# Performance work log

Measured on AMD Instinct MI355X. Metric: run time of the kernel, lower is better.

## Reference

```python
import jax, jax.numpy as jnp
import numpy as np

HEAD_NUM = 16
EMBED = 1024

def setup_inputs() -> dict:
    key = jax.random.key(0)
    k1, k2, k3 = jax.random.split(key, 3)
    x = jax.random.normal(k1, (2, 2048, EMBED), dtype=jnp.float32)
    W_qkv = jax.random.normal(k2, (3 * EMBED, EMBED), dtype=jnp.float32) * (EMBED ** -0.5)
    W_out = jax.random.normal(k3, (EMBED, EMBED), dtype=jnp.float32) * (EMBED ** -0.5)
    return {"x": x, "W_qkv": W_qkv, "W_out": W_out}

def reference(x, W_qkv, W_out):
    b, t, E = x.shape
    h = HEAD_NUM
    d = E // h
    dk = (E / h) ** 0.5
    qkv = x @ W_qkv.T  # [b, t, 3E]
    # einops 'b t (d k h) -> k b h t d' with k=3, h=head_num (d outermost in the split)
    qkv = qkv.reshape(b, t, d, 3, h).transpose(3, 0, 4, 1, 2)  # [3, b, h, t, d]
    q, k, v = qkv[0], qkv[1], qkv[2]
    energy = jnp.einsum('bhid,bhjd->bhij', q, k) / dk  # [b, h, t, t]
    attn = jax.nn.softmax(energy, axis=-1)
    out = jnp.einsum('bhij,bhjd->bhid', attn, v)  # [b, h, t, d]
    out = out.transpose(0, 2, 1, 3).reshape(b, t, E)  # 'b h t d -> b t (h d)'
    return out @ W_out.T
```

## Files before the change

### kernel.cpp

```cpp
#include <hip/hip_runtime.h>
#include <hip/hip_bf16.h>


#define HEADS 16
#define EMB   1024
#define HDIM  64
#define BB    2
#define TT    2048
#define QSCALE 0.18033688011112042f

typedef __attribute__((ext_vector_type(8)))  short      bf16x8;
typedef __attribute__((ext_vector_type(8)))  _Float16   f16x8;
typedef __attribute__((ext_vector_type(4)))  float      f32x4;
typedef __attribute__((ext_vector_type(16))) float      f32x16;
typedef __attribute__((ext_vector_type(4)))  unsigned   u32x4;

__device__ __forceinline__ unsigned short f2bf(float f) {
    __hip_bfloat16 h = __float2bfloat16(f);
    return __builtin_bit_cast(unsigned short, h);
}
__device__ __forceinline__ float fexp2(float x) {
#if __has_builtin(__builtin_amdgcn_exp2f)
    return __builtin_amdgcn_exp2f(x);
#else
    return exp2f(x);
#endif
}
__device__ __forceinline__ unsigned pkrtz(float a, float b) {
    auto r = __builtin_amdgcn_cvt_pkrtz(a, b);
    return __builtin_bit_cast(unsigned, r);
}
__device__ __forceinline__ unsigned short f2h(float f) {
    return (unsigned short)(pkrtz(f, 0.f) & 0xffffu);
}
__device__ __forceinline__ float h2f(unsigned short u) {
    return (float)__builtin_bit_cast(_Float16, u);
}
__device__ __forceinline__ void gload_lds16(const void* g, void* l) {
    __builtin_amdgcn_global_load_lds(
        (const __attribute__((address_space(1))) void*)g,
        (__attribute__((address_space(3))) void*)l, 16, 0, 0);
}
__device__ __forceinline__ int swzi(int row, int blk) {
    return row * 64 + ((blk ^ (row & 7)) << 3);
}
__device__ __forceinline__ void pl32swap(unsigned& a, unsigned& b) {
    asm("v_permlane32_swap_b32 %0, %1" : "+v"(a), "+v"(b));
}

__global__ __launch_bounds__(256)
void conv_bf16(const float* __restrict__ src, unsigned short* __restrict__ dst,
               int n8) {
    int i = blockIdx.x * 256 + threadIdx.x;
    if (i >= n8) return;
    const float4 v0 = ((const float4*)src)[i * 2];
    const float4 v1 = ((const float4*)src)[i * 2 + 1];
    ushort4 a, b;
    a.x = f2bf(v0.x); a.y = f2bf(v0.y); a.z = f2bf(v0.z); a.w = f2bf(v0.w);
    b.x = f2bf(v1.x); b.y = f2bf(v1.y); b.z = f2bf(v1.z); b.w = f2bf(v1.w);
    ((ushort4*)dst)[i * 2]     = a;
    ((ushort4*)dst)[i * 2 + 1] = b;
}

template<int PERM>
__global__ __launch_bounds__(256)
void convw(const float* __restrict__ src, unsigned short* __restrict__ dst) {
    const int np = blockIdx.x;
    const int ns = PERM ? ((np & 63) * 48 + (np >> 10) * 16 + ((np >> 6) & 15))
                        : np;
    const float4 v = ((const float4*)(src + (size_t)ns * 1024))[threadIdx.x];
    ushort4 u;
    u.x = f2bf(v.x); u.y = f2bf(v.y); u.z = f2bf(v.z); u.w = f2bf(v.w);
    ((ushort4*)(dst + (size_t)np * 1024))[threadIdx.x] = u;
}

template<int EPI>
__global__ __launch_bounds__(256)
void gemm_bf16(const unsigned short* __restrict__ Ag,
               const unsigned short* __restrict__ Wg,
               float* __restrict__ Cout,
               unsigned short* __restrict__ QKb,
               unsigned short* __restrict__ Vt) {
    __shared__ __align__(16) unsigned short Ab[128 * 64];
    __shared__ __align__(16) unsigned short Wb[128 * 64];

    const int tid = threadIdx.x, lane = tid & 63, w = tid >> 6;
    const int n0 = blockIdx.x * 128, m0 = blockIdx.y * 128;
    const int wn = (w >> 1) * 64, wm = (w & 1) * 64;
    const int r16 = lane & 15, g = lane >> 4;

    f32x4 acc[4][4];
    #pragma unroll
    for (int i = 0; i < 4; ++i)
        #pragma unroll
        for (int j = 0; j < 4; ++j)
            acc[i][j] = (f32x4){0.f, 0.f, 0.f, 0.f};

    const int srl = lane >> 3;
    const int scb = lane & 7;

    for (int kt = 0; kt < 16; ++kt) {
        __syncthreads();
        const int k0 = kt * 64;
        #pragma unroll
        for (int i = 0; i < 4; ++i) {
            const int row = w * 32 + i * 8 + srl;
            const int cbs = (scb ^ (row & 7)) << 3;
            gload_lds16(Ag + (size_t)(m0 + row) * 1024 + k0 + cbs,
                        Ab + (size_t)(w * 32 + i * 8) * 64);
            gload_lds16(Wg + (size_t)(n0 + row) * 1024 + k0 + cbs,
                        Wb + (size_t)(w * 32 + i * 8) * 64);
        }
        __syncthreads();

        #pragma unroll
        for (int ks = 0; ks < 2; ++ks) {
            bf16x8 xf[4];
            #pragma unroll
            for (int mi = 0; mi < 4; ++mi)
                xf[mi] = *(const bf16x8*)&Ab[swzi(wm + mi * 16 + r16, ks * 4 + g)];
            #pragma unroll
            for (int ni = 0; ni < 4; ++ni) {
                const bf16x8 wf = *(const bf16x8*)&Wb[swzi(wn + ni * 16 + r16, ks * 4 + g)];
                #pragma unroll
                for (int mi = 0; mi < 4; ++mi)
                    acc[ni][mi] = __builtin_amdgcn_mfma_f32_16x16x32_bf16(
                        wf, xf[mi], acc[ni][mi], 0, 0, 0);
            }
        }
    }

    const int gq = g * 4;
    if (EPI == 0) {
        #pragma unroll
        for (int ni = 0; ni < 4; ++ni)
            #pragma unroll
            for (int mi = 0; mi < 4; ++mi) {
                const int m = m0 + wm + mi * 16 + r16;
                *(f32x4*)&Cout[(size_t)m * 1024 + (n0 + wn + ni * 16 + gq)] =
                    acc[ni][mi];
            }
    } else if (n0 < 2048) {
        #pragma unroll
        for (int ni = 0; ni < 4; ++ni) {
            const float qs = (n0 + wn + ni * 16) < 1024 ? QSCALE : 1.0f;
            #pragma unroll
            for (int mi = 0; mi < 4; ++mi) {
                const int m  = m0 + wm + mi * 16 + r16;
                const int np = n0 + wn + ni * 16 + gq;
                ushort4 u;
                u.x = f2bf(acc[ni][mi][0] * qs); u.y = f2bf(acc[ni][mi][1] * qs);
                u.z = f2bf(acc[ni][mi][2] * qs); u.w = f2bf(acc[ni][mi][3] * qs);
                *(ushort4*)&QKb[(size_t)m * 2048 + np] = u;
            }
        }
    } else {
        const int b = m0 >> 11, t0 = m0 & 2047;
        #pragma unroll
        for (int ni = 0; ni < 4; ++ni)
            #pragma unroll
            for (int mi = 0; mi < 4; ++mi) {
                const int t   = t0 + wm + mi * 16 + r16;
                const int nv0 = (n0 - 2048) + wn + ni * 16 + gq;
                #pragma unroll
                for (int j = 0; j < 4; ++j) {
                    const int nv = nv0 + j, h = nv >> 6, d = nv & 63;
                    Vt[(((size_t)(b * HEADS + h)) * HDIM + d) * TT + t] =
                        f2h(acc[ni][mi][j]);
                }
            }
    }
}

__global__ __launch_bounds__(256)
void attn32(const unsigned short* __restrict__ QKb,
            const unsigned short* __restrict__ Vt,
            unsigned short* __restrict__ PO0,
            unsigned short* __restrict__ PO1,
            float* __restrict__ PL0,
            float* __restrict__ PL1) {
    __shared__ __align__(16) unsigned short Ks[2][64 * 64];
    __shared__ __align__(16) unsigned short Vs[2][64 * 64];

    const int tid = threadIdx.x, lane = tid & 63, w = tid >> 6;
    const int l31 = lane & 31, hi = lane >> 5;
    const int qt = blockIdx.x & 15, kh = blockIdx.x >> 4;
    const int h = blockIdx.y, b = blockIdx.z;
    const int kbase = kh * 1024;
    const unsigned short* Vsrc = Vt + (size_t)(b * HEADS + h) * HDIM * TT;
    unsigned short* PO = kh ? PO1 : PO0;
    float*          PL = kh ? PL1 : PL0;

    bf16x8 qf[4];
    {
        const unsigned short* qrow =
            QKb + ((size_t)(b * TT + qt * 128 + w * 32 + l31)) * 2048 + h * HDIM;
        #pragma unroll
        for (int dc = 0; dc < 4; ++dc)
            qf[dc] = *(const bf16x8*)(qrow + dc * 16 + hi * 8);
    }

    const f32x16 zz = {};
    f32x16 o0 = {}, o1 = {};
    float lrun = 0.f;

    const int srl = lane >> 3;
    const int scb = lane & 7;

#define STAGEKV(BUF, J0)                                                         \
    do {                                                                         \
        _Pragma("unroll")                                                        \
        for (int i = 0; i < 2; ++i) {                                            \
            const int rl  = w * 16 + i * 8 + srl;                                \
            const int cbs = (scb ^ (rl & 7)) << 3;                               \
            gload_lds16(QKb + (size_t)(b * TT + (J0) + rl) * 2048 + 1024 +       \
                            h * HDIM + cbs,                                      \
                        &Ks[BUF][(w * 16 + i * 8) * 64]);                        \
            gload_lds16(Vsrc + (size_t)rl * TT + (J0) + cbs,                     \
                        &Vs[BUF][(w * 16 + i * 8) * 64]);                        \
        }                                                                        \
    } while (0)

    STAGEKV(0, kbase);

    for (int jt = 0; jt < 16; ++jt) {
        const int bb = jt & 1;
        __syncthreads();
        if (jt < 15) STAGEKV(bb ^ 1, kbase + (jt + 1) * 64);

        f32x16 st0, st1;
        __builtin_amdgcn_s_setprio(1);
        #pragma unroll
        for (int dc = 0; dc < 4; ++dc) {
            const bf16x8 ka0 = *(const bf16x8*)&Ks[bb][swzi(l31,      dc * 2 + hi)];
            const bf16x8 ka1 = *(const bf16x8*)&Ks[bb][swzi(32 + l31, dc * 2 + hi)];
            if (dc == 0) {
                st0 = __builtin_amdgcn_mfma_f32_32x32x16_bf16(ka0, qf[0], zz, 0, 0, 0);
                st1 = __builtin_amdgcn_mfma_f32_32x32x16_bf16(ka1, qf[0], zz, 0, 0, 0);
            } else {
                st0 = __builtin_amdgcn_mfma_f32_32x32x16_bf16(ka0, qf[dc], st0, 0, 0, 0);
                st1 = __builtin_amdgcn_mfma_f32_32x32x16_bf16(ka1, qf[dc], st1, 0, 0, 0);
            }
        }
        __builtin_amdgcn_s_setprio(0);

        float p[32];
        #pragma unroll
        for (int j = 0; j < 16; ++j) {
            p[j]      = fexp2(st0[j]);
            p[16 + j] = fexp2(st1[j]);
        }
        {
            float t[16];
            #pragma unroll
            for (int j = 0; j < 16; ++j) t[j] = p[j] + p[16 + j];
            #pragma unroll
            for (int j = 0; j < 8; ++j) t[j] += t[j + 8];
            #pragma unroll
            for (int j = 0; j < 4; ++j) t[j] += t[j + 4];
            lrun += (t[0] + t[1]) + (t[2] + t[3]);
        }

        unsigned wd[16];
        #pragma unroll
        for (int c = 0; c < 4; ++c) {
            wd[c * 2 + 0]     = pkrtz(p[4 * c + 0],      p[4 * c + 1]);
            wd[c * 2 + 1]     = pkrtz(p[4 * c + 2],      p[4 * c + 3]);
            wd[8 + c * 2 + 0] = pkrtz(p[16 + 4 * c + 0], p[16 + 4 * c + 1]);
            wd[8 + c * 2 + 1] = pkrtz(p[16 + 4 * c + 2], p[16 + 4 * c + 3]);
        }
        f16x8 pa[4];
        #pragma unroll
        for (int f = 0; f < 4; ++f) {
            unsigned w0 = wd[f * 4 + 0], w2 = wd[f * 4 + 2];
            pl32swap(w0, w2);
            unsigned w1 = wd[f * 4 + 1], w3 = wd[f * 4 + 3];
            pl32swap(w1, w3);
            const u32x4 fv = {w0, w1, w2, w3};
            pa[f] = __builtin_bit_cast(f16x8, fv);
        }

        __builtin_amdgcn_s_setprio(1);
        #pragma unroll
        for (int f = 0; f < 4; ++f) {
            const f16x8 vb0 = *(const f16x8*)&Vs[bb][swzi(l31,      f * 2 + hi)];
            const f16x8 vb1 = *(const f16x8*)&Vs[bb][swzi(32 + l31, f * 2 + hi)];
            o0 = __builtin_amdgcn_mfma_f32_32x32x16_f16(pa[f], vb0, o0, 0, 0, 0);
            o1 = __builtin_amdgcn_mfma_f32_32x32x16_f16(pa[f], vb1, o1, 0, 0, 0);
        }
        __builtin_amdgcn_s_setprio(0);
    }
#undef STAGEKV

    lrun += __shfl_xor(lrun, 32);
    const float inv = 1.0f / lrun;
    #pragma unroll
    for (int r = 0; r < 16; ++r) {
        const int qr = (r & 3) + 8 * (r >> 2) + 4 * hi;
        const float ir = __shfl(inv, qr);
        const int q = qt * 128 + w * 32 + qr;
        unsigned short* dst = PO + ((size_t)(b * TT + q)) * EMB + h * HDIM + l31;
        dst[0]  = f2h(o0[r] * ir);
        dst[32] = f2h(o1[r] * ir);
    }
    if (!hi) {
        const int q = qt * 128 + w * 32 + l31;
        PL[((size_t)(b * HEADS + h)) * TT + q] = lrun;
    }
}

__global__ __launch_bounds__(256)
void merge_attn(const unsigned short* __restrict__ PO0,
                const unsigned short* __restrict__ PO1,
                const float* __restrict__ PL0,
                const float* __restrict__ PL1,
                unsigned short* __restrict__ AOb) {
    const int i = blockIdx.x * 256 + threadIdx.x;
    const int tg  = i >> 8;
    const int col = (i & 255) * 4;
    const int h   = col >> 6;
    const int b   = tg >> 11, t = tg & 2047;

    const float la = PL0[((size_t)(b * HEADS + h)) * TT + t];
    const float lb = PL1[((size_t)(b * HEADS + h)) * TT + t];
    const float inv = 1.0f / (la + lb);
    const float wa = la * inv, wb = lb * inv;

    const ushort4 a = ((const ushort4*)PO0)[i];
    const ushort4 c = ((const ushort4*)PO1)[i];
    ushort4 o;
    o.x = f2bf(h2f(a.x) * wa + h2f(c.x) * wb);
    o.y = f2bf(h2f(a.y) * wa + h2f(c.y) * wb);
    o.z = f2bf(h2f(a.z) * wa + h2f(c.z) * wb);
    o.w = f2bf(h2f(a.w) * wa + h2f(c.w) * wb);
    ((ushort4*)AOb)[i] = o;
}

extern "C" void kernel_launch(void* const* d_in, const int* in_sizes, int n_in,
                              void* d_out, int out_size, void* d_ws, size_t ws_size,
                              hipStream_t stream) {
    const float* x    = (const float*)d_in[0];
    const float* Wqkv = (const float*)d_in[1];
    const float* Wout = (const float*)d_in[2];
    float* out = (float*)d_out;

    unsigned short* Wqb = (unsigned short*)d_ws;
    unsigned short* Wob = Wqb + 3145728;
    unsigned short* xb  = Wob + 1048576;
    unsigned short* QKb = xb  + 4194304;
    unsigned short* Vt  = QKb + 8388608;
    unsigned short* PO0 = Vt  + 4194304;
    unsigned short* PO1 = PO0 + 4194304;
    float*          PL0 = (float*)(PO1 + 4194304);
    float*          PL1 = PL0 + 65536;
    unsigned short* AOb = xb;

    conv_bf16<<<2048, 256, 0, stream>>>(x, xb, 524288);
    convw<1><<<3072, 256, 0, stream>>>(Wqkv, Wqb);
    convw<0><<<1024, 256, 0, stream>>>(Wout, Wob);

    gemm_bf16<1><<<dim3(24, 32), 256, 0, stream>>>(xb, Wqb, nullptr, QKb, Vt);

    attn32<<<dim3(32, 16, 2), 256, 0, stream>>>(QKb, Vt, PO0, PO1, PL0, PL1);

    merge_attn<<<4096, 256, 0, stream>>>(PO0, PO1, PL0, PL1, AOb);

    gemm_bf16<0><<<dim3(8, 32), 256, 0, stream>>>(AOb, Wob, out, nullptr, nullptr);
}
```

Measured before the change: 143.4 us.

## Hoist staging pointers, split softmax-PV per half, raise occupancy hint

The attention kernel now precomputes its K/V global and LDS staging addresses once and advances them by a constant stride, instead of recomputing swizzled addresses every tile. The exp/pack/PV stage is split into two halves (one per 32-key score block), so each half's PV MFMAs can start sooner and fewer probability values are live at once. The launch bounds now request 4 blocks per SM to cap register use. The intent is lower address arithmetic and register pressure and better overlap of exp with MFMA; the cap risks spills or the compiler reordering the schedule differently.

```diff
diff --git a/kernel.cpp b/kernel.cpp
--- a/kernel.cpp
+++ b/kernel.cpp
@@ -172,7 +172,7 @@
     }
 }
 
-__global__ __launch_bounds__(256)
+__global__ __launch_bounds__(256, 4)
 void attn32(const unsigned short* __restrict__ QKb,
             const unsigned short* __restrict__ Vt,
             unsigned short* __restrict__ PO0,
@@ -206,91 +206,95 @@
 
     const int srl = lane >> 3;
     const int scb = lane & 7;
-
-#define STAGEKV(BUF, J0)                                                         \
-    do {                                                                         \
-        _Pragma("unroll")                                                        \
-        for (int i = 0; i < 2; ++i) {                                            \
-            const int rl  = w * 16 + i * 8 + srl;                                \
-            const int cbs = (scb ^ (rl & 7)) << 3;                               \
-            gload_lds16(QKb + (size_t)(b * TT + (J0) + rl) * 2048 + 1024 +       \
-                            h * HDIM + cbs,                                      \
-                        &Ks[BUF][(w * 16 + i * 8) * 64]);                        \
-            gload_lds16(Vsrc + (size_t)rl * TT + (J0) + cbs,                     \
-                        &Vs[BUF][(w * 16 + i * 8) * 64]);                        \
-        }                                                                        \
+    const int cbs = (scb ^ srl) << 3;
+    const int rl0 = w * 16 + srl, rl1 = rl0 + 8;
+    const unsigned short* kp0 =
+        QKb + (size_t)(b * TT + kbase + rl0) * 2048 + 1024 + h * HDIM + cbs;
+    const unsigned short* kp1 = kp0 + (size_t)8 * 2048;
+    const unsigned short* vp0 = Vsrc + (size_t)rl0 * TT + kbase + cbs;
+    const unsigned short* vp1 = vp0 + (size_t)8 * TT;
+    unsigned short* const kd0 = &Ks[0][(w * 16) * 64];
+    unsigned short* const kd1 = &Ks[1][(w * 16) * 64];
+    unsigned short* const vd0 = &Vs[0][(w * 16) * 64];
+    unsigned short* const vd1 = &Vs[1][(w * 16) * 64];
+
+#define STAGE(KD, VD)                                                  \
+    do {                                                               \
+        gload_lds16(kp0, (KD));        gload_lds16(kp1, (KD) + 512);   \
+        gload_lds16(vp0, (VD));        gload_lds16(vp1, (VD) + 512);   \
+        kp0 += 64 * 2048; kp1 += 64 * 2048; vp0 += 64; vp1 += 64;      \
     } while (0)
 
-    STAGEKV(0, kbase);
+    STAGE(kd0, vd0);
 
     for (int jt = 0; jt < 16; ++jt) {
         const int bb = jt & 1;
         __syncthreads();
-        if (jt < 15) STAGEKV(bb ^ 1, kbase + (jt + 1) * 64);
-
-        f32x16 st0, st1;
+        if (jt < 15) {
+            if (bb) STAGE(kd0, vd0); else STAGE(kd1, vd1);
+        }
+        const unsigned short* KsB = &Ks[bb][0];
+        const unsigned short* VsB = &Vs[bb][0];
+
+        f32x16 stA, stB;
         __builtin_amdgcn_s_setprio(1);
         #pragma unroll
         for (int dc = 0; dc < 4; ++dc) {
-            const bf16x8 ka0 = *(const bf16x8*)&Ks[bb][swzi(l31,      dc * 2 + hi)];
-            const bf16x8 ka1 = *(const bf16x8*)&Ks[bb][swzi(32 + l31, dc * 2 + hi)];
+            const bf16x8 kaA = *(const bf16x8*)&KsB[swzi(l31,      dc * 2 + hi)];
+            const bf16x8 kaB = *(const bf16x8*)&KsB[swzi(32 + l31, dc * 2 + hi)];
             if (dc == 0) {
-                st0 = __builtin_amdgcn_mfma_f32_32x32x16_bf16(ka0, qf[0], zz, 0, 0, 0);
-                st1 = __builtin_amdgcn_mfma_f32_32x32x16_bf16(ka1, qf[0], zz, 0, 0, 0);
+                stA = __builtin_amdgcn_mfma_f32_32x32x16_bf16(kaA, qf[0], zz, 0, 0, 0);
+                stB = __builtin_amdgcn_mfma_f32_32x32x16_bf16(kaB, qf[0], zz, 0, 0, 0);
             } else {
-                st0 = __builtin_amdgcn_mfma_f32_32x32x16_bf16(ka0, qf[dc], st0, 0, 0, 0);
-                st1 = __builtin_amdgcn_mfma_f32_32x32x16_bf16(ka1, qf[dc], st1, 0, 0, 0);
+                stA = __builtin_amdgcn_mfma_f32_32x32x16_bf16(kaA, qf[dc], stA, 0, 0, 0);
+                stB = __builtin_amdgcn_mfma_f32_32x32x16_bf16(kaB, qf[dc], stB, 0, 0, 0);
             }
         }
         __builtin_amdgcn_s_setprio(0);
 
-        float p[32];
-        #pragma unroll
-        for (int j = 0; j < 16; ++j) {
-            p[j]      = fexp2(st0[j]);
-            p[16 + j] = fexp2(st1[j]);
-        }
-        {
-            float t[16];
-            #pragma unroll
-            for (int j = 0; j < 16; ++j) t[j] = p[j] + p[16 + j];
-            #pragma unroll
-            for (int j = 0; j < 8; ++j) t[j] += t[j + 8];
-            #pragma unroll
-            for (int j = 0; j < 4; ++j) t[j] += t[j + 4];
-            lrun += (t[0] + t[1]) + (t[2] + t[3]);
-        }
-
-        unsigned wd[16];
-        #pragma unroll
-        for (int c = 0; c < 4; ++c) {
-            wd[c * 2 + 0]     = pkrtz(p[4 * c + 0],      p[4 * c + 1]);
-            wd[c * 2 + 1]     = pkrtz(p[4 * c + 2],      p[4 * c + 3]);
-            wd[8 + c * 2 + 0] = pkrtz(p[16 + 4 * c + 0], p[16 + 4 * c + 1]);
-            wd[8 + c * 2 + 1] = pkrtz(p[16 + 4 * c + 2], p[16 + 4 * c + 3]);
-        }
-        f16x8 pa[4];
-        #pragma unroll
-        for (int f = 0; f < 4; ++f) {
-            unsigned w0 = wd[f * 4 + 0], w2 = wd[f * 4 + 2];
-            pl32swap(w0, w2);
-            unsigned w1 = wd[f * 4 + 1], w3 = wd[f * 4 + 3];
-            pl32swap(w1, w3);
-            const u32x4 fv = {w0, w1, w2, w3};
-            pa[f] = __builtin_bit_cast(f16x8, fv);
-        }
-
-        __builtin_amdgcn_s_setprio(1);
-        #pragma unroll
-        for (int f = 0; f < 4; ++f) {
-            const f16x8 vb0 = *(const f16x8*)&Vs[bb][swzi(l31,      f * 2 + hi)];
-            const f16x8 vb1 = *(const f16x8*)&Vs[bb][swzi(32 + l31, f * 2 + hi)];
-            o0 = __builtin_amdgcn_mfma_f32_32x32x16_f16(pa[f], vb0, o0, 0, 0, 0);
-            o1 = __builtin_amdgcn_mfma_f32_32x32x16_f16(pa[f], vb1, o1, 0, 0, 0);
-        }
-        __builtin_amdgcn_s_setprio(0);
-    }
-#undef STAGEKV
+        #pragma unroll
+        for (int x = 0; x < 2; ++x) {
+            const f32x16& st = x ? stB : stA;
+            float sum;
+            unsigned wd[8];
+            #pragma unroll
+            for (int c = 0; c < 4; ++c) {
+                const float e0 = fexp2(st[4 * c + 0]);
+                const float e1 = fexp2(st[4 * c + 1]);
+                const float e2 = fexp2(st[4 * c + 2]);
+                const float e3 = fexp2(st[4 * c + 3]);
+                const float s4 = (e0 + e1) + (e2 + e3);
+                sum = c ? sum + s4 : s4;
+                wd[2 * c]     = pkrtz(e0, e1);
+                wd[2 * c + 1] = pkrtz(e2, e3);
+            }
+            lrun += sum;
+
+            unsigned a0 = wd[0], a2 = wd[2];  pl32swap(a0, a2);
+            unsigned a1 = wd[1], a3 = wd[3];  pl32swap(a1, a3);
+            unsigned b0 = wd[4], b2 = wd[6];  pl32swap(b0, b2);
+            unsigned b1 = wd[5], b3 = wd[7];  pl32swap(b1, b3);
+            const u32x4 fa = {a0, a1, a2, a3};
+            const u32x4 fb = {b0, b1, b2, b3};
+            const f16x8 pa0 = __builtin_bit_cast(f16x8, fa);
+            const f16x8 pa1 = __builtin_bit_cast(f16x8, fb);
+
+            const int f0 = 2 * x;
+            __builtin_amdgcn_s_setprio(1);
+            {
+                const f16x8 vb00 = *(const f16x8*)&VsB[swzi(l31,      f0 * 2 + hi)];
+                const f16x8 vb01 = *(const f16x8*)&VsB[swzi(32 + l31, f0 * 2 + hi)];
+                o0 = __builtin_amdgcn_mfma_f32_32x32x16_f16(pa0, vb00, o0, 0, 0, 0);
+                o1 = __builtin_amdgcn_mfma_f32_32x32x16_f16(pa0, vb01, o1, 0, 0, 0);
+                const f16x8 vb10 = *(const f16x8*)&VsB[swzi(l31,      (f0 + 1) * 2 + hi)];
+                const f16x8 vb11 = *(const f16x8*)&VsB[swzi(32 + l31, (f0 + 1) * 2 + hi)];
+                o0 = __builtin_amdgcn_mfma_f32_32x32x16_f16(pa1, vb10, o0, 0, 0, 0);
+                o1 = __builtin_amdgcn_mfma_f32_32x32x16_f16(pa1, vb11, o1, 0, 0, 0);
+            }
+            __builtin_amdgcn_s_setprio(0);
+        }
+    }
+#undef STAGE
 
     lrun += __shfl_xor(lrun, 32);
     const float inv = 1.0f / lrun;
```

New measurement: 134.3 us. -6.3%, faster.
